# Kernel optimization log

Measured on AMD Instinct MI355X. Metric: run time of the kernel, lower is better.

Reference implementation:

```python
import jax, jax.numpy as jnp
import numpy as np

N_QUBITS = 10
N_LAYERS = 2
QSVT_DEGREE = 3
DT_RANK = 5  # n_qubits // 2
PI = np.float32(np.pi)

# ---- batched statevector simulation helpers (wire 0 = most significant, as in pennylane default.qubit) ----

def _apply_1q(s, wire, U):
    # s: (batch,) + (2,)*n complex; U: (batch,2,2) or (2,2)
    s = jnp.moveaxis(s, 1 + wire, 1)
    shp = s.shape
    s2 = s.reshape(shp[0], 2, -1)
    if U.ndim == 3:
        out = jnp.einsum('bij,bjr->bir', U, s2)
    else:
        out = jnp.einsum('ij,bjr->bir', U, s2)
    return jnp.moveaxis(out.reshape(shp), 1, 1 + wire)

def _ry(t):
    c = jnp.cos(t / 2).astype(jnp.complex64)
    s = jnp.sin(t / 2).astype(jnp.complex64)
    return jnp.stack([jnp.stack([c, -s], -1), jnp.stack([s, c], -1)], -2)

def _rz(t):
    e = jnp.exp(-0.5j * jnp.asarray(t).astype(jnp.complex64))
    z = jnp.zeros_like(e)
    return jnp.stack([jnp.stack([e, z], -1), jnp.stack([z, jnp.conj(e)], -1)], -2)

def _rx(t):
    c = jnp.cos(t / 2).astype(jnp.complex64)
    s = (-1j) * jnp.sin(t / 2).astype(jnp.complex64)
    return jnp.stack([jnp.stack([c, s], -1), jnp.stack([s, c], -1)], -2)

def _cnot(s, control, target):
    f = jnp.flip(s, axis=1 + target)
    s0 = jax.lax.index_in_dim(s, 0, axis=1 + control, keepdims=True)
    f1 = jax.lax.index_in_dim(f, 1, axis=1 + control, keepdims=True)
    return jnp.concatenate([s0, f1], axis=1 + control)

def _circuit(h, x, dt, cp, pc):
    """Batched selective QSVT circuit; h,x,dt: (B,n). Returns <Z_i> per wire, (B,n) float32."""
    n = N_QUBITS
    b = h.shape[0]
    s = jnp.zeros((b, 2 ** n), jnp.complex64).at[:, 0].set(1.0).reshape((b,) + (2,) * n)
    # 1. state encoding
    for i in range(n):
        s = _apply_1q(s, i, _ry(h[:, i]))
    # 2. delta-modulated QSVT block
    for d in range(QSVT_DEGREE + 1):
        for i in range(n):
            s = _apply_1q(s, i, _rz(pc[d] * dt[:, i] * PI))
        for i in range(n - 1):
            s = _cnot(s, i, i + 1)
        s = _cnot(s, n - 1, 0)
    # 3. variational block
    k = 0
    for _ in range(N_LAYERS):
        for i in range(n):
            s = _apply_1q(s, i, _rx(cp[k]))
            s = _apply_1q(s, i, _ry(cp[k + 1]))
            s = _apply_1q(s, i, _rz(cp[k + 2]))
            k += 3
        for i in range(n - 1):
            s = _cnot(s, i, i + 1)
    # 4. delta-modulated input encoding
    for i in range(n):
        s = _apply_1q(s, i, _ry(x[:, i] * dt[:, i]))
    # 5. <Z_i> measurements
    p = s.real ** 2 + s.imag ** 2
    zs = [(jax.lax.index_in_dim(p, 0, 1 + i, False) - jax.lax.index_in_dim(p, 1, 1 + i, False)).reshape(b, -1).sum(-1) for i in range(n)]
    return jnp.stack(zs, -1).astype(jnp.float32)

def setup_inputs() -> dict:
    key = jax.random.key(0)
    ks = jax.random.split(key, 6)
    B, S, n, r = 128, 512, N_QUBITS, DT_RANK
    angles = jax.random.uniform(ks[0], (B, S, n), jnp.float32) * PI  # angle encoding in [0, pi]
    W_x = jax.random.normal(ks[1], (r + 2 * n, n), jnp.float32) * 0.3  # x_proj weight (no bias)
    W_dt = jax.random.normal(ks[2], (n, r), jnp.float32) * 0.3  # dt_proj weight
    rng = np.random.default_rng(0)
    dt0 = np.exp(rng.random(n) * (np.log(0.1) - np.log(0.001)) + np.log(0.001))
    b_dt = jnp.asarray(dt0 + np.log(-np.expm1(-dt0)), jnp.float32)  # inverse-softplus init
    poly_coeffs = jax.random.normal(ks[3], (QSVT_DEGREE + 1,), jnp.float32) * 0.1
    circuit_params = jax.random.normal(ks[4], (n * N_LAYERS * 3,), jnp.float32) * 0.1
    D = jnp.ones((n,), jnp.float32)
    return {"angles": angles, "W_x": W_x, "W_dt": W_dt, "b_dt": b_dt,
            "poly_coeffs": poly_coeffs, "circuit_params": circuit_params, "D": D}

def reference(angles, W_x, W_dt, b_dt, poly_coeffs, circuit_params, D):
    # selective projections
    x_dbc = jnp.einsum('bsn,kn->bsk', angles, W_x)
    dt_raw = x_dbc[..., :DT_RANK]
    # B slice (x_dbc[..., DT_RANK:DT_RANK+n]) is computed but unused in the original forward
    C = x_dbc[..., DT_RANK + N_QUBITS:]
    dt = jax.nn.softplus(jnp.einsum('bsr,nr->bsn', dt_raw, W_dt) + b_dt)
    dt_angles = jnp.tanh(dt) * PI
    # quantum recurrence uses detached tensors in the original (torch .detach())
    x_sg = jax.lax.stop_gradient(angles)
    dt_sg = jax.lax.stop_gradient(dt_angles)
    cp = jax.lax.stop_gradient(circuit_params)
    pc = jax.lax.stop_gradient(poly_coeffs)

    def step(h, xs):
        x_t, d_t = xs
        h2 = _circuit(h, x_t, d_t, cp, pc)
        return h2, h2

    h0 = jnp.zeros((angles.shape[0], N_QUBITS), jnp.float32)
    _, hs = jax.lax.scan(step, h0, (jnp.swapaxes(x_sg, 0, 1), jnp.swapaxes(dt_sg, 0, 1)))
    hs = jnp.swapaxes(hs, 0, 1)  # (B,S,n)
    return C * hs + D * angles
```

## Files before the change

kernel.cpp:

```cpp
#include <hip/hip_runtime.h>
#include <math.h>


#define PIF 3.14159265358979323846f

constexpr int NQ = 10, SEQ = 512, NB = 128, NTHR = 512, RECF = 36;

struct CTbl { int mz[4][NQ]; };
constexpr CTbl build_tbl() {
  CTbl t{};
  unsigned mrow[NQ];
  for (int b = 0; b < NQ; ++b) mrow[b] = 1u << b;
  for (int d = 0; d < 4; ++d) {
    for (int i = 0; i < NQ; ++i) t.mz[d][i] = (int)mrow[9 - i];
    for (int i = 0; i < NQ - 1; ++i) { int bc = 9 - i, bt = 8 - i; mrow[bt] ^= mrow[bc]; }
    mrow[9] ^= mrow[0];
  }
  return t;
}
constexpr CTbl CT = build_tbl();

struct PermCols { int c4[10]; int cL[10]; };
constexpr PermCols build_perms() {
  PermCols P{};
  for (int b = 0; b < 10; ++b) {
    int x = 1 << b;
    for (int d = 0; d < 4; ++d) {
      for (int i = 0; i < 9; ++i) { int bc = 9 - i, bt = 8 - i; if ((x >> bc) & 1) x ^= (1 << bt); }
      if (x & 1) x ^= (1 << 9);
    }
    P.c4[b] = x;
    int y = 1 << b;
    for (int i = 0; i < 9; ++i) { int bc = 9 - i, bt = 8 - i; if ((y >> bc) & 1) y ^= (1 << bt); }
    P.cL[b] = y;
  }
  return P;
}
constexpr PermCols PC = build_perms();

constexpr int lanePart(int x)  { return ((x >> 0) & 1) | (((x >> 5) & 1) << 1) |
                                        (((x >> 1) & 1) << 2) | (((x >> 7) & 1) << 3) |
                                        (((x >> 3) & 1) << 4) | (((x >> 9) & 1) << 5); }
constexpr int wavePart8(int x) { return ((x >> 4) & 1) | (((x >> 8) & 1) << 1) |
                                        (((x >> 6) & 1) << 2); }

typedef __attribute__((ext_vector_type(2))) float v2;

constexpr int VOFS[8] = {0, 16, 256, 272, 64, 80, 320, 336};

template<int C>
__device__ __forceinline__ int dpp1(int x) {
  return __builtin_amdgcn_update_dpp(x, x, C, 0xF, 0xF, false);
}
template<int VL>
__device__ __forceinline__ int lxi(int x) {
  if constexpr (VL == 1)  return dpp1<0xB1>(x);
  else if constexpr (VL == 2)  return dpp1<0x4E>(x);
  else if constexpr (VL == 3)  return dpp1<0x1B>(x);
  else if constexpr (VL <= 7) {
    constexpr int q = (VL & 3) ^ 3;
    int y = x;
    if constexpr (q == 1) y = dpp1<0xB1>(y);
    else if constexpr (q == 2) y = dpp1<0x4E>(y);
    else if constexpr (q == 3) y = dpp1<0x1B>(y);
    return dpp1<0x141>(y);
  } else if constexpr (VL >= 12) {
    constexpr int q = (VL & 3) ^ 3;
    int y = x;
    if constexpr (q == 1) y = dpp1<0xB1>(y);
    else if constexpr (q == 2) y = dpp1<0x4E>(y);
    else if constexpr (q == 3) y = dpp1<0x1B>(y);
    return dpp1<0x140>(y);
  } else {
    constexpr int a = VL & 3;
    int y = x;
    if constexpr (a == 1) y = dpp1<0xB1>(y);
    else if constexpr (a == 2) y = dpp1<0x4E>(y);
    else if constexpr (a == 3) y = dpp1<0x1B>(y);
    y = dpp1<0x141>(y);
    return dpp1<0x140>(y);
  }
}
template<int VL>
__device__ __forceinline__ float lx(float x) {
  if constexpr (VL == 0) return x;
  else if constexpr (VL & 32) {
    int addr = (((int)threadIdx.x & 63) ^ VL) << 2;
    return __int_as_float(__builtin_amdgcn_ds_bpermute(addr, __float_as_int(x)));
  } else if constexpr (VL & 16) {
    return __int_as_float(__builtin_amdgcn_ds_swizzle(__float_as_int(x), (VL << 10) | 0x1F));
  } else {
    return __int_as_float(lxi<VL>(__float_as_int(x)));
  }
}
__device__ __forceinline__ float rdl(float x, int l) {
  return __int_as_float(__builtin_amdgcn_readlane(__float_as_int(x), l));
}

__device__ __forceinline__ int swz(int j) {
  return j ^ (((j >> 5) & 1) << 2) ^ ((j >> 7) & 1);
}

__device__ __forceinline__ void apply2(v2* amp, const v2* p, bool par, float4 U0, float4 U1) {
  v2 u00 = {U0.x, U0.y}, u01 = {U0.z, U0.w}, u10 = {U1.x, U1.y}, u11 = {U1.z, U1.w};
  v2 A = par ? u11 : u00, B = par ? u10 : u01;
  v2 An = {-A.y, A.y}, Bn = {-B.y, B.y};
#pragma unroll
  for (int r = 0; r < 2; ++r) {
    v2 o = amp[r], q = p[r];
    v2 res = A.x * o;
    res += An * __builtin_shufflevector(o, o, 1, 0);
    res += B.x * q;
    res += Bn * __builtin_shufflevector(q, q, 1, 0);
    amp[r] = res;
  }
}

template<int VL>
__device__ __forceinline__ void gate_lane2(v2* amp, float4 U0, float4 U1, int lane) {
  v2 p[2];
#pragma unroll
  for (int r = 0; r < 2; ++r) { p[r].x = lx<VL>(amp[r].x); p[r].y = lx<VL>(amp[r].y); }
  apply2(amp, p, (lane & VL) != 0, U0, U1);
}

__device__ __forceinline__ void gate_reg1(v2* amp, float4 U0, float4 U1) {
  v2 u00 = {U0.x, U0.y}, u01 = {U0.z, U0.w}, u10 = {U1.x, U1.y}, u11 = {U1.z, U1.w};
  v2 o0 = amp[0], o1 = amp[1];
  v2 a0 = {0.f, 0.f}, a1 = {0.f, 0.f};
  a0.x += u00.x * o0.x - u00.y * o0.y;  a0.y += u00.x * o0.y + u00.y * o0.x;
  a0.x += u01.x * o1.x - u01.y * o1.y;  a0.y += u01.x * o1.y + u01.y * o1.x;
  a1.x += u10.x * o0.x - u10.y * o0.y;  a1.y += u10.x * o0.y + u10.y * o0.x;
  a1.x += u11.x * o1.x - u11.y * o1.y;  a1.y += u11.x * o1.y + u11.y * o1.x;
  amp[0] = a0; amp[1] = a1;
}

template<int VL>
__device__ __forceinline__ float xdot_lane2(const v2* amp) {
  v2 acc = {0.f, 0.f};
#pragma unroll
  for (int r = 0; r < 2; ++r) {
    v2 p; p.x = lx<VL>(amp[r].x); p.y = lx<VL>(amp[r].y);
    acc += amp[r] * p;
  }
  return acc.x + acc.y;
}

__global__ __launch_bounds__(NTHR, 2) void qmamba_main(
    const float* __restrict__ angles, const float* __restrict__ Wx,
    const float* __restrict__ Wdt, const float* __restrict__ bdt,
    const float* __restrict__ pc, const float* __restrict__ cp,
    float* __restrict__ out)
{
  __shared__ float  tblL[SEQ][RECF];
  __shared__ float4 uuL[40];
  __shared__ v2     ex0[1024];
  __shared__ v2     ex1[1024];
  __shared__ float  zb[8][16];

  const int tid  = threadIdx.x;
  const int lane = tid & 63;
  const int wave = tid >> 6;
  const int b    = blockIdx.x;

  if (tid < 20) {
    int k = tid * 3;
    float al = 0.5f * cp[k], be = 0.5f * cp[k + 1], ga = 0.5f * cp[k + 2];
    float ca = __cosf(al), sa = __sinf(al);
    float cb = __cosf(be), sb = __sinf(be);
    float cg = __cosf(ga), sg = __sinf(ga);
    float2 M00 = make_float2(cb * ca,  sb * sa);
    float2 M01 = make_float2(-sb * ca, -cb * sa);
    float2 M10 = make_float2(sb * ca,  -cb * sa);
    float2 M11 = make_float2(cb * ca,  -sb * sa);
    float2 e0 = make_float2(cg, -sg), e1 = make_float2(cg, sg);
    auto cm = [](float2 a, float2 c) {
      return make_float2(a.x * c.x - a.y * c.y, a.x * c.y + a.y * c.x);
    };
    float2 u00 = cm(M00, e0), u01 = cm(M01, e0), u10 = cm(M10, e1), u11 = cm(M11, e1);
    uuL[2 * tid]     = make_float4(u00.x, u00.y, u01.x, u01.y);
    uuL[2 * tid + 1] = make_float4(u10.x, u10.y, u11.x, u11.y);
  }

  {
    const int t = tid;
    const float* ar = angles + (size_t)(b * SEQ + t) * NQ;
    float a[NQ];
#pragma unroll
    for (int n = 0; n < NQ; ++n) a[n] = ar[n];
    float dtr[5];
#pragma unroll
    for (int r = 0; r < 5; ++r) {
      float acc = 0.f;
#pragma unroll
      for (int n = 0; n < NQ; ++n) acc += a[n] * Wx[r * NQ + n];
      dtr[r] = acc;
    }
    float* rec = &tblL[t][0];
#pragma unroll
    for (int w = 0; w < NQ; ++w) {
      float lin = bdt[w];
#pragma unroll
      for (int r = 0; r < 5; ++r) lin += dtr[r] * Wdt[w * 5 + r];
      float sp = lin > 0.f ? lin + log1pf(__expf(-lin)) : log1pf(__expf(lin));
      float th = tanhf(sp) * PIF;
      float fa = a[w] * th;
      rec[w]      = th;
      rec[12 + w] = __cosf(fa);
      rec[24 + w] = __sinf(fa);
    }
  }
  __syncthreads();

  float pch[4];
#pragma unroll
  for (int d = 0; d < 4; ++d) pch[d] = 0.5f * pc[d] * PIF;

  v2 cw0[8], cw1[8];
  {
    const int s5 = wave & 1, s1 = (wave >> 1) & 1, s3 = (wave >> 2) & 1;
    auto ent = [&](int g, int row, int col) -> v2 {
      float4 R = uuL[2 * g + row];
      return col ? v2{R.z, R.w} : v2{R.x, R.y};
    };
    auto cmul = [](v2 a, v2 c) -> v2 {
      return v2{a.x * c.x - a.y * c.y, a.x * c.y + a.y * c.x};
    };
#pragma unroll
    for (int v = 0; v < 8; ++v) {
      const int v5 = v & 1, v1 = (v >> 1) & 1, v3 = (v >> 2) & 1;
      cw0[v] = cmul(cmul(ent(5,  s5, s5 ^ v5), ent(1,  s1, s1 ^ v1)), ent(3,  s3, s3 ^ v3));
      cw1[v] = cmul(cmul(ent(15, s5, s5 ^ v5), ent(11, s1, s1 ^ v1)), ent(13, s3, s3 ^ v3));
    }
  }

  unsigned PW0 = 0, PW1 = 0;
#pragma unroll
  for (int k = 0; k < 40; ++k) {
    const int m  = CT.mz[k / 10][k % 10];
    const int lm = lanePart(m), wm = wavePart8(m);
    unsigned flip = ((unsigned)((__popc(lane & lm) ^ __popc(wave & wm)) & 1)) ^ 1u;
    if (k < 32) PW0 |= flip << k; else PW1 |= flip << (k - 32);
  }

  int d4 = 0, dL = 0;
  if (lane & 1)  { d4 ^= PC.c4[0]; dL ^= PC.cL[0]; }
  if (lane & 2)  { d4 ^= PC.c4[5]; dL ^= PC.cL[5]; }
  if (lane & 4)  { d4 ^= PC.c4[1]; dL ^= PC.cL[1]; }
  if (lane & 8)  { d4 ^= PC.c4[7]; dL ^= PC.cL[7]; }
  if (lane & 16) { d4 ^= PC.c4[3]; dL ^= PC.cL[3]; }
  if (lane & 32) { d4 ^= PC.c4[9]; dL ^= PC.cL[9]; }
  if (wave & 1)  { d4 ^= PC.c4[4]; dL ^= PC.cL[4]; }
  if (wave & 2)  { d4 ^= PC.c4[8]; dL ^= PC.cL[8]; }
  if (wave & 4)  { d4 ^= PC.c4[6]; dL ^= PC.cL[6]; }
  const int oR4 = PC.c4[2], oRL = PC.cL[2];

  const int oidx = (lane & 1) | (((lane >> 1) & 1) << 5) | (((lane >> 2) & 1) << 1)
                 | (((lane >> 3) & 1) << 7) | (((lane >> 4) & 1) << 3) | (((lane >> 5) & 1) << 9)
                 | ((wave & 1) << 4) | (((wave >> 1) & 1) << 8) | (((wave >> 2) & 1) << 6);

  float hcw[NQ], hsw[NQ];
#pragma unroll
  for (int w = 0; w < NQ; ++w) { hcw[w] = 1.f; hsw[w] = 0.f; }

  v2 amp[2];

#pragma unroll 1
  for (int t = 0; t < SEQ; ++t) {
    float tha[12];
    {
      const float4* rq = (const float4*)&tblL[t][0];
#pragma unroll
      for (int j = 0; j < 3; ++j) ((float4*)tha)[j] = rq[j];
    }

    float F;
    F  = (lane & 1)  ? hsw[9] : hcw[9];
    F *= (lane & 2)  ? hsw[4] : hcw[4];
    F *= (lane & 4)  ? hsw[8] : hcw[8];
    F *= (lane & 8)  ? hsw[2] : hcw[2];
    F *= (lane & 16) ? hsw[6] : hcw[6];
    F *= (lane & 32) ? hsw[0] : hcw[0];
    F *= (wave & 1)  ? hsw[5] : hcw[5];
    F *= (wave & 2)  ? hsw[1] : hcw[1];
    F *= (wave & 4)  ? hsw[3] : hcw[3];
    const float G0 = F * hcw[7];
    const float G1 = F * hsw[7];

    float S0 = 0.f, S1 = 0.f;
#pragma unroll
    for (int k = 0; k < 40; ++k) {
      const int m  = CT.mz[k / 10][k % 10];
      float v = pch[k / 10] * tha[k % 10];
      unsigned fl = ((k < 32 ? (PW0 >> k) : (PW1 >> (k - 32))) & 1u) << 31;
      float sv = __int_as_float(__float_as_int(v) ^ fl);
      if ((m >> 2) & 1) S1 += sv; else S0 += sv;
    }
    {
      float sn, cs;
      __sincosf(S0 + S1, &sn, &cs); amp[0].x = G0 * cs; amp[0].y = G0 * sn;
      __sincosf(S0 - S1, &sn, &cs); amp[1].x = G1 * cs; amp[1].y = G1 * sn;
    }

    ex0[swz(d4)]       = amp[0];
    ex0[swz(d4 ^ oR4)] = amp[1];
    __syncthreads();
    {
      v2 pv0[8], pv1[8];
#pragma unroll
      for (int v = 0; v < 8; ++v) {
        const int base = oidx ^ VOFS[v];
        pv0[v] = ex0[swz(base)];
        pv1[v] = ex0[swz(base | 4)];
      }
      v2 a0 = {0.f, 0.f}, a1 = {0.f, 0.f};
#pragma unroll
      for (int v = 0; v < 8; ++v) {
        v2 c = cw0[v];
        a0.x += c.x * pv0[v].x - c.y * pv0[v].y;
        a0.y += c.x * pv0[v].y + c.y * pv0[v].x;
        a1.x += c.x * pv1[v].x - c.y * pv1[v].y;
        a1.y += c.x * pv1[v].y + c.y * pv1[v].x;
      }
      amp[0] = a0; amp[1] = a1;
    }
    gate_lane2<32>(amp, uuL[0],  uuL[1],  lane);
    gate_lane2<8> (amp, uuL[4],  uuL[5],  lane);
    gate_lane2<2> (amp, uuL[8],  uuL[9],  lane);
    gate_lane2<16>(amp, uuL[12], uuL[13], lane);
    gate_reg1     (amp, uuL[14], uuL[15]);
    gate_lane2<4> (amp, uuL[16], uuL[17], lane);
    gate_lane2<1> (amp, uuL[18], uuL[19], lane);

    ex1[swz(dL)]       = amp[0];
    ex1[swz(dL ^ oRL)] = amp[1];
    __syncthreads();
    {
      v2 pv0[8], pv1[8];
#pragma unroll
      for (int v = 0; v < 8; ++v) {
        const int base = oidx ^ VOFS[v];
        pv0[v] = ex1[swz(base)];
        pv1[v] = ex1[swz(base | 4)];
      }
      v2 a0 = {0.f, 0.f}, a1 = {0.f, 0.f};
#pragma unroll
      for (int v = 0; v < 8; ++v) {
        v2 c = cw1[v];
        a0.x += c.x * pv0[v].x - c.y * pv0[v].y;
        a0.y += c.x * pv0[v].y + c.y * pv0[v].x;
        a1.x += c.x * pv1[v].x - c.y * pv1[v].y;
        a1.y += c.x * pv1[v].y + c.y * pv1[v].x;
      }
      amp[0] = a0; amp[1] = a1;
    }
    gate_lane2<32>(amp, uuL[20], uuL[21], lane);
    gate_lane2<8> (amp, uuL[24], uuL[25], lane);
    gate_lane2<2> (amp, uuL[28], uuL[29], lane);
    gate_lane2<16>(amp, uuL[32], uuL[33], lane);
    gate_reg1     (amp, uuL[34], uuL[35]);
    gate_lane2<4> (amp, uuL[36], uuL[37], lane);
    gate_lane2<1> (amp, uuL[38], uuL[39], lane);

    ex0[swz(dL)]       = amp[0];
    ex0[swz(dL ^ oRL)] = amp[1];
    __syncthreads();
    v2 pw5[2], pw1[2], pw3[2];
    amp[0] = ex0[swz(oidx)];
    amp[1] = ex0[swz(oidx | 4)];
    pw5[0] = ex0[swz(oidx ^ 16)];   pw5[1] = ex0[swz((oidx ^ 16) | 4)];
    pw1[0] = ex0[swz(oidx ^ 256)];  pw1[1] = ex0[swz((oidx ^ 256) | 4)];
    pw3[0] = ex0[swz(oidx ^ 64)];   pw3[1] = ex0[swz((oidx ^ 64) | 4)];

    float cfv[12], sfv[12];
    {
      const float4* rq = (const float4*)&tblL[t][0];
#pragma unroll
      for (int j = 0; j < 3; ++j) { ((float4*)cfv)[j] = rq[3 + j]; ((float4*)sfv)[j] = rq[6 + j]; }
    }

    const float n0 = amp[0].x * amp[0].x + amp[0].y * amp[0].y;
    const float n1 = amp[1].x * amp[1].x + amp[1].y * amp[1].y;
    const float T0 = n0 + n1;
    const float T1 = n0 - n1;

    auto vdot2 = [](const v2* a, const v2* p) {
      v2 acc = a[0] * p[0] + a[1] * p[1];
      return acc.x + acc.y;
    };

    float zv[NQ];
    { float zp = (lane & 32) ? -T0 : T0; zv[0] = cfv[0] * zp - sfv[0] * xdot_lane2<32>(amp); }
    { float zp = (wave & 2)  ? -T0 : T0; zv[1] = cfv[1] * zp - sfv[1] * vdot2(amp, pw1); }
    { float zp = (lane & 8)  ? -T0 : T0; zv[2] = cfv[2] * zp - sfv[2] * xdot_lane2<8>(amp); }
    { float zp = (wave & 4)  ? -T0 : T0; zv[3] = cfv[3] * zp - sfv[3] * vdot2(amp, pw3); }
    { float zp = (lane & 2)  ? -T0 : T0; zv[4] = cfv[4] * zp - sfv[4] * xdot_lane2<2>(amp); }
    { float zp = (wave & 1)  ? -T0 : T0; zv[5] = cfv[5] * zp - sfv[5] * vdot2(amp, pw5); }
    { float zp = (lane & 16) ? -T0 : T0; zv[6] = cfv[6] * zp - sfv[6] * xdot_lane2<16>(amp); }
    { float xr = 2.f * (amp[0].x * amp[1].x + amp[0].y * amp[1].y);
      zv[7] = cfv[7] * T1 - sfv[7] * xr; }
    { float zp = (lane & 4)  ? -T0 : T0; zv[8] = cfv[8] * zp - sfv[8] * xdot_lane2<4>(amp); }
    { float zp = (lane & 1)  ? -T0 : T0; zv[9] = cfv[9] * zp - sfv[9] * xdot_lane2<1>(amp); }

#pragma unroll
    for (int w = 0; w < NQ; ++w) {
      zv[w] += lx<1>(zv[w]);
      zv[w] += lx<2>(zv[w]);
      zv[w] += lx<4>(zv[w]);
    }
    const int l7 = lane & 7;
    float c01 = (l7 & 1) ? zv[1] : zv[0];
    float c23 = (l7 & 1) ? zv[3] : zv[2];
    float c45 = (l7 & 1) ? zv[5] : zv[4];
    float c67 = (l7 & 1) ? zv[7] : zv[6];
    float c03 = (l7 & 2) ? c23 : c01;
    float c47 = (l7 & 2) ? c67 : c45;
    float pk  = (l7 & 4) ? c47 : c03;
    pk += lx<8>(pk);  pk += lx<16>(pk);  pk += lx<32>(pk);
    float z8 = zv[8]; z8 += lx<8>(z8); z8 += lx<16>(z8); z8 += lx<32>(z8);
    float z9 = zv[9]; z9 += lx<8>(z9); z9 += lx<16>(z9); z9 += lx<32>(z9);
    float zsel = pk;
    zsel = (lane == 8) ? z8 : zsel;
    zsel = (lane == 9) ? z9 : zsel;

    if (lane < NQ) zb[wave][lane] = zsel;
    __syncthreads();
    float z = 0.f;
    if (lane < NQ) {
      z = zb[0][lane] + zb[1][lane] + zb[2][lane] + zb[3][lane]
        + zb[4][lane] + zb[5][lane] + zb[6][lane] + zb[7][lane];
      if (wave == 0) out[(size_t)(b * SEQ + t) * NQ + lane] = z;
    }
    float sn_h, cs_h;
    __sincosf(0.5f * z, &sn_h, &cs_h);
#pragma unroll
    for (int w = 0; w < NQ; ++w) { hcw[w] = rdl(cs_h, w); hsw[w] = rdl(sn_h, w); }
  }
}

__global__ __launch_bounds__(256) void qmamba_post(
    const float* __restrict__ angles, const float* __restrict__ Wx,
    const float* __restrict__ Dg, float* __restrict__ out)
{
  int i = blockIdx.x * 256 + threadIdx.x;
  if (i >= NB * SEQ * NQ) return;
  int w  = i % NQ;
  int bt = i / NQ;
  const float* a = angles + (size_t)bt * NQ;
  float C = 0.f;
#pragma unroll
  for (int n = 0; n < NQ; ++n) C += a[n] * Wx[(15 + w) * NQ + n];
  float z = out[i];
  out[i] = C * z + Dg[w] * a[w];
}

extern "C" void kernel_launch(void* const* d_in, const int* in_sizes, int n_in,
                              void* d_out, int out_size, void* d_ws, size_t ws_size,
                              hipStream_t stream) {
  (void)in_sizes; (void)n_in; (void)out_size; (void)d_ws; (void)ws_size;
  const float* angles = (const float*)d_in[0];
  const float* Wx     = (const float*)d_in[1];
  const float* Wdt    = (const float*)d_in[2];
  const float* bdt    = (const float*)d_in[3];
  const float* pc     = (const float*)d_in[4];
  const float* cp     = (const float*)d_in[5];
  const float* Dg     = (const float*)d_in[6];
  float* out = (float*)d_out;
  hipLaunchKernelGGL(qmamba_main, dim3(NB), dim3(NTHR), 0, stream,
                     angles, Wx, Wdt, bdt, pc, cp, out);
  hipLaunchKernelGGL(qmamba_post, dim3((NB * SEQ * NQ + 255) / 256), dim3(256), 0, stream,
                     angles, Wx, Dg, out);
}
```

Baseline: 2.221 ms.

## Pack two batch elements per block and remap LDS exchange to float4 reads

Each block now runs two independent batch elements with 1024 threads (64 blocks instead of 128), each half using its own LDS exchange buffers and reduction slots. The shared-memory exchange layout is remapped with a new bit permutation and swizzle, so every thread reads both of its amplitudes with a single float4 load instead of two v2 loads. The per-step table is packed tighter (30 floats per step) and read as float2. Intent is fewer LDS instructions per step; the cost is that block-wide barriers now also stall the other element's waves, and there are fewer blocks to spread across CUs.

Result: slower. 7.337 ms (+230.3%).

```diff
diff --git a/kernel.cpp b/kernel.cpp
--- a/kernel.cpp
+++ b/kernel.cpp
@@ -4,7 +4,7 @@
 
 #define PIF 3.14159265358979323846f
 
-constexpr int NQ = 10, SEQ = 512, NB = 128, NTHR = 512, RECF = 36;
+constexpr int NQ = 10, SEQ = 512, NBATCH = 128, NTHR = 1024, NBLK = 64;
 
 struct CTbl { int mz[4][NQ]; };
 constexpr CTbl build_tbl() {
@@ -44,9 +44,18 @@
 constexpr int wavePart8(int x) { return ((x >> 4) & 1) | (((x >> 8) & 1) << 1) |
                                         (((x >> 6) & 1) << 2); }
 
+constexpr int kmap(int x) {
+  return ((x >> 2) & 1)
+       | (((x >> 0) & 1) << 1) | (((x >> 5) & 1) << 2) | (((x >> 1) & 1) << 3)
+       | (((x >> 7) & 1) << 4) | (((x >> 3) & 1) << 5) | (((x >> 9) & 1) << 6)
+       | (((x >> 4) & 1) << 7) | (((x >> 8) & 1) << 8) | (((x >> 6) & 1) << 9);
+}
+constexpr int swzk(int k) { return k ^ (((k >> 5) & 1) << 1) ^ (((k >> 4) & 1) << 2); }
+
+constexpr int SKC4 = swzk(kmap(PC.c4[2]));
+constexpr int SKCL = swzk(kmap(PC.cL[2]));
+
 typedef __attribute__((ext_vector_type(2))) float v2;
-
-constexpr int VOFS[8] = {0, 16, 256, 272, 64, 80, 320, 336};
 
 template<int C>
 __device__ __forceinline__ int dpp1(int x) {
@@ -97,10 +106,6 @@
   return __int_as_float(__builtin_amdgcn_readlane(__float_as_int(x), l));
 }
 
-__device__ __forceinline__ int swz(int j) {
-  return j ^ (((j >> 5) & 1) << 2) ^ ((j >> 7) & 1);
-}
-
 __device__ __forceinline__ void apply2(v2* amp, const v2* p, bool par, float4 U0, float4 U1) {
   v2 u00 = {U0.x, U0.y}, u01 = {U0.z, U0.w}, u10 = {U1.x, U1.y}, u11 = {U1.z, U1.w};
   v2 A = par ? u11 : u00, B = par ? u10 : u01;
@@ -127,11 +132,11 @@
 __device__ __forceinline__ void gate_reg1(v2* amp, float4 U0, float4 U1) {
   v2 u00 = {U0.x, U0.y}, u01 = {U0.z, U0.w}, u10 = {U1.x, U1.y}, u11 = {U1.z, U1.w};
   v2 o0 = amp[0], o1 = amp[1];
-  v2 a0 = {0.f, 0.f}, a1 = {0.f, 0.f};
-  a0.x += u00.x * o0.x - u00.y * o0.y;  a0.y += u00.x * o0.y + u00.y * o0.x;
-  a0.x += u01.x * o1.x - u01.y * o1.y;  a0.y += u01.x * o1.y + u01.y * o1.x;
-  a1.x += u10.x * o0.x - u10.y * o0.y;  a1.y += u10.x * o0.y + u10.y * o0.x;
-  a1.x += u11.x * o1.x - u11.y * o1.y;  a1.y += u11.x * o1.y + u11.y * o1.x;
+  v2 a0, a1;
+  a0.x = u00.x * o0.x - u00.y * o0.y + u01.x * o1.x - u01.y * o1.y;
+  a0.y = u00.x * o0.y + u00.y * o0.x + u01.x * o1.y + u01.y * o1.x;
+  a1.x = u10.x * o0.x - u10.y * o0.y + u11.x * o1.x - u11.y * o1.y;
+  a1.y = u10.x * o0.y + u10.y * o0.x + u11.x * o1.y + u11.y * o1.x;
   amp[0] = a0; amp[1] = a1;
 }
 
@@ -146,22 +151,23 @@
   return acc.x + acc.y;
 }
 
-__global__ __launch_bounds__(NTHR, 2) void qmamba_main(
+__global__ __launch_bounds__(NTHR) void qmamba_main(
     const float* __restrict__ angles, const float* __restrict__ Wx,
     const float* __restrict__ Wdt, const float* __restrict__ bdt,
     const float* __restrict__ pc, const float* __restrict__ cp,
     float* __restrict__ out)
 {
-  __shared__ float  tblL[SEQ][RECF];
+  __shared__ __align__(16) float tbl[2][SEQ][30];
   __shared__ float4 uuL[40];
-  __shared__ v2     ex0[1024];
-  __shared__ v2     ex1[1024];
-  __shared__ float  zb[8][16];
+  __shared__ __align__(16) v2 ex[2][2][1024];
+  __shared__ float  zb[2][8][16];
 
   const int tid  = threadIdx.x;
   const int lane = tid & 63;
   const int wave = tid >> 6;
-  const int b    = blockIdx.x;
+  const int el   = wave >> 3;
+  const int wv   = wave & 7;
+  const int bel  = blockIdx.x * 2 + el;
 
   if (tid < 20) {
     int k = tid * 3;
@@ -183,8 +189,9 @@
   }
 
   {
-    const int t = tid;
-    const float* ar = angles + (size_t)(b * SEQ + t) * NQ;
+    const int pel = tid >> 9, t = tid & (SEQ - 1);
+    const int pb  = blockIdx.x * 2 + pel;
+    const float* ar = angles + (size_t)(pb * SEQ + t) * NQ;
     float a[NQ];
 #pragma unroll
     for (int n = 0; n < NQ; ++n) a[n] = ar[n];
@@ -196,7 +203,7 @@
       for (int n = 0; n < NQ; ++n) acc += a[n] * Wx[r * NQ + n];
       dtr[r] = acc;
     }
-    float* rec = &tblL[t][0];
+    float* rec = &tbl[pel][t][0];
 #pragma unroll
     for (int w = 0; w < NQ; ++w) {
       float lin = bdt[w];
@@ -206,8 +213,8 @@
       float th = tanhf(sp) * PIF;
       float fa = a[w] * th;
       rec[w]      = th;
-      rec[12 + w] = __cosf(fa);
-      rec[24 + w] = __sinf(fa);
+      rec[10 + w] = __cosf(fa);
+      rec[20 + w] = __sinf(fa);
     }
   }
   __syncthreads();
@@ -218,7 +225,7 @@
 
   v2 cw0[8], cw1[8];
   {
-    const int s5 = wave & 1, s1 = (wave >> 1) & 1, s3 = (wave >> 2) & 1;
+    const int s5 = wv & 1, s1 = (wv >> 1) & 1, s3 = (wv >> 2) & 1;
     auto ent = [&](int g, int row, int col) -> v2 {
       float4 R = uuL[2 * g + row];
       return col ? v2{R.z, R.w} : v2{R.x, R.y};
@@ -239,25 +246,26 @@
   for (int k = 0; k < 40; ++k) {
     const int m  = CT.mz[k / 10][k % 10];
     const int lm = lanePart(m), wm = wavePart8(m);
-    unsigned flip = ((unsigned)((__popc(lane & lm) ^ __popc(wave & wm)) & 1)) ^ 1u;
+    unsigned flip = ((unsigned)((__popc(lane & lm) ^ __popc(wv & wm)) & 1)) ^ 1u;
     if (k < 32) PW0 |= flip << k; else PW1 |= flip << (k - 32);
   }
 
-  int d4 = 0, dL = 0;
-  if (lane & 1)  { d4 ^= PC.c4[0]; dL ^= PC.cL[0]; }
-  if (lane & 2)  { d4 ^= PC.c4[5]; dL ^= PC.cL[5]; }
-  if (lane & 4)  { d4 ^= PC.c4[1]; dL ^= PC.cL[1]; }
-  if (lane & 8)  { d4 ^= PC.c4[7]; dL ^= PC.cL[7]; }
-  if (lane & 16) { d4 ^= PC.c4[3]; dL ^= PC.cL[3]; }
-  if (lane & 32) { d4 ^= PC.c4[9]; dL ^= PC.cL[9]; }
-  if (wave & 1)  { d4 ^= PC.c4[4]; dL ^= PC.cL[4]; }
-  if (wave & 2)  { d4 ^= PC.c4[8]; dL ^= PC.cL[8]; }
-  if (wave & 4)  { d4 ^= PC.c4[6]; dL ^= PC.cL[6]; }
-  const int oR4 = PC.c4[2], oRL = PC.cL[2];
-
-  const int oidx = (lane & 1) | (((lane >> 1) & 1) << 5) | (((lane >> 2) & 1) << 1)
-                 | (((lane >> 3) & 1) << 7) | (((lane >> 4) & 1) << 3) | (((lane >> 5) & 1) << 9)
-                 | ((wave & 1) << 4) | (((wave >> 1) & 1) << 8) | (((wave >> 2) & 1) << 6);
+  int d4k = 0, dLk = 0;
+  if (lane & 1)  { d4k ^= kmap(PC.c4[0]); dLk ^= kmap(PC.cL[0]); }
+  if (lane & 2)  { d4k ^= kmap(PC.c4[5]); dLk ^= kmap(PC.cL[5]); }
+  if (lane & 4)  { d4k ^= kmap(PC.c4[1]); dLk ^= kmap(PC.cL[1]); }
+  if (lane & 8)  { d4k ^= kmap(PC.c4[7]); dLk ^= kmap(PC.cL[7]); }
+  if (lane & 16) { d4k ^= kmap(PC.c4[3]); dLk ^= kmap(PC.cL[3]); }
+  if (lane & 32) { d4k ^= kmap(PC.c4[9]); dLk ^= kmap(PC.cL[9]); }
+  if (wv & 1)    { d4k ^= kmap(PC.c4[4]); dLk ^= kmap(PC.cL[4]); }
+  if (wv & 2)    { d4k ^= kmap(PC.c4[8]); dLk ^= kmap(PC.cL[8]); }
+  if (wv & 4)    { d4k ^= kmap(PC.c4[6]); dLk ^= kmap(PC.cL[6]); }
+  const int sd4  = swzk(d4k);
+  const int sdL  = swzk(dLk);
+  const int sown = swzk((lane << 1) | (wv << 7));
+
+  v2* const exA = &ex[el][0][0];
+  v2* const exB = &ex[el][1][0];
 
   float hcw[NQ], hsw[NQ];
 #pragma unroll
@@ -267,11 +275,11 @@
 
 #pragma unroll 1
   for (int t = 0; t < SEQ; ++t) {
-    float tha[12];
-    {
-      const float4* rq = (const float4*)&tblL[t][0];
-#pragma unroll
-      for (int j = 0; j < 3; ++j) ((float4*)tha)[j] = rq[j];
+    float thv[10];
+    {
+      const float2* rq = (const float2*)&tbl[el][t][0];
+#pragma unroll
+      for (int j = 0; j < 5; ++j) { float2 q = rq[j]; thv[2 * j] = q.x; thv[2 * j + 1] = q.y; }
     }
 
     float F;
@@ -281,9 +289,9 @@
     F *= (lane & 8)  ? hsw[2] : hcw[2];
     F *= (lane & 16) ? hsw[6] : hcw[6];
     F *= (lane & 32) ? hsw[0] : hcw[0];
-    F *= (wave & 1)  ? hsw[5] : hcw[5];
-    F *= (wave & 2)  ? hsw[1] : hcw[1];
-    F *= (wave & 4)  ? hsw[3] : hcw[3];
+    F *= (wv & 1)    ? hsw[5] : hcw[5];
+    F *= (wv & 2)    ? hsw[1] : hcw[1];
+    F *= (wv & 4)    ? hsw[3] : hcw[3];
     const float G0 = F * hcw[7];
     const float G1 = F * hsw[7];
 
@@ -291,7 +299,7 @@
 #pragma unroll
     for (int k = 0; k < 40; ++k) {
       const int m  = CT.mz[k / 10][k % 10];
-      float v = pch[k / 10] * tha[k % 10];
+      float v = pch[k / 10] * thv[k % 10];
       unsigned fl = ((k < 32 ? (PW0 >> k) : (PW1 >> (k - 32))) & 1u) << 31;
       float sv = __int_as_float(__float_as_int(v) ^ fl);
       if ((m >> 2) & 1) S1 += sv; else S0 += sv;
@@ -302,25 +310,18 @@
       __sincosf(S0 - S1, &sn, &cs); amp[1].x = G1 * cs; amp[1].y = G1 * sn;
     }
 
-    ex0[swz(d4)]       = amp[0];
-    ex0[swz(d4 ^ oR4)] = amp[1];
+    exA[sd4]        = amp[0];
+    exA[sd4 ^ SKC4] = amp[1];
     __syncthreads();
     {
-      v2 pv0[8], pv1[8];
+      const float4* q4 = (const float4*)exA;
+      v2 a0 = {0.f, 0.f}, a1 = {0.f, 0.f};
 #pragma unroll
       for (int v = 0; v < 8; ++v) {
-        const int base = oidx ^ VOFS[v];
-        pv0[v] = ex0[swz(base)];
-        pv1[v] = ex0[swz(base | 4)];
-      }
-      v2 a0 = {0.f, 0.f}, a1 = {0.f, 0.f};
-#pragma unroll
-      for (int v = 0; v < 8; ++v) {
+        float4 q = q4[(sown ^ (v << 7)) >> 1];
         v2 c = cw0[v];
-        a0.x += c.x * pv0[v].x - c.y * pv0[v].y;
-        a0.y += c.x * pv0[v].y + c.y * pv0[v].x;
-        a1.x += c.x * pv1[v].x - c.y * pv1[v].y;
-        a1.y += c.x * pv1[v].y + c.y * pv1[v].x;
+        a0.x += c.x * q.x - c.y * q.y;  a0.y += c.x * q.y + c.y * q.x;
+        a1.x += c.x * q.z - c.y * q.w;  a1.y += c.x * q.w + c.y * q.z;
       }
       amp[0] = a0; amp[1] = a1;
     }
@@ -332,25 +333,18 @@
     gate_lane2<4> (amp, uuL[16], uuL[17], lane);
     gate_lane2<1> (amp, uuL[18], uuL[19], lane);
 
-    ex1[swz(dL)]       = amp[0];
-    ex1[swz(dL ^ oRL)] = amp[1];
+    exB[sdL]        = amp[0];
+    exB[sdL ^ SKCL] = amp[1];
     __syncthreads();
     {
-      v2 pv0[8], pv1[8];
+      const float4* q4 = (const float4*)exB;
+      v2 a0 = {0.f, 0.f}, a1 = {0.f, 0.f};
 #pragma unroll
       for (int v = 0; v < 8; ++v) {
-        const int base = oidx ^ VOFS[v];
-        pv0[v] = ex1[swz(base)];
-        pv1[v] = ex1[swz(base | 4)];
-      }
-      v2 a0 = {0.f, 0.f}, a1 = {0.f, 0.f};
-#pragma unroll
-      for (int v = 0; v < 8; ++v) {
+        float4 q = q4[(sown ^ (v << 7)) >> 1];
         v2 c = cw1[v];
-        a0.x += c.x * pv0[v].x - c.y * pv0[v].y;
-        a0.y += c.x * pv0[v].y + c.y * pv0[v].x;
-        a1.x += c.x * pv1[v].x - c.y * pv1[v].y;
-        a1.y += c.x * pv1[v].y + c.y * pv1[v].x;
+        a0.x += c.x * q.x - c.y * q.y;  a0.y += c.x * q.y + c.y * q.x;
+        a1.x += c.x * q.z - c.y * q.w;  a1.y += c.x * q.w + c.y * q.z;
       }
       amp[0] = a0; amp[1] = a1;
     }
@@ -362,21 +356,31 @@
     gate_lane2<4> (amp, uuL[36], uuL[37], lane);
     gate_lane2<1> (amp, uuL[38], uuL[39], lane);
 
-    ex0[swz(dL)]       = amp[0];
-    ex0[swz(dL ^ oRL)] = amp[1];
+    exA[sdL]        = amp[0];
+    exA[sdL ^ SKCL] = amp[1];
     __syncthreads();
     v2 pw5[2], pw1[2], pw3[2];
-    amp[0] = ex0[swz(oidx)];
-    amp[1] = ex0[swz(oidx | 4)];
-    pw5[0] = ex0[swz(oidx ^ 16)];   pw5[1] = ex0[swz((oidx ^ 16) | 4)];
-    pw1[0] = ex0[swz(oidx ^ 256)];  pw1[1] = ex0[swz((oidx ^ 256) | 4)];
-    pw3[0] = ex0[swz(oidx ^ 64)];   pw3[1] = ex0[swz((oidx ^ 64) | 4)];
-
-    float cfv[12], sfv[12];
-    {
-      const float4* rq = (const float4*)&tblL[t][0];
-#pragma unroll
-      for (int j = 0; j < 3; ++j) { ((float4*)cfv)[j] = rq[3 + j]; ((float4*)sfv)[j] = rq[6 + j]; }
+    {
+      const float4* q4 = (const float4*)exA;
+      float4 qs = q4[sown >> 1];
+      float4 q5 = q4[(sown ^ (1 << 7)) >> 1];
+      float4 q1 = q4[(sown ^ (2 << 7)) >> 1];
+      float4 q3 = q4[(sown ^ (4 << 7)) >> 1];
+      amp[0] = v2{qs.x, qs.y}; amp[1] = v2{qs.z, qs.w};
+      pw5[0] = v2{q5.x, q5.y}; pw5[1] = v2{q5.z, q5.w};
+      pw1[0] = v2{q1.x, q1.y}; pw1[1] = v2{q1.z, q1.w};
+      pw3[0] = v2{q3.x, q3.y}; pw3[1] = v2{q3.z, q3.w};
+    }
+
+    float cfv[10], sfv[10];
+    {
+      const float2* rq = (const float2*)&tbl[el][t][0];
+#pragma unroll
+      for (int j = 0; j < 5; ++j) {
+        float2 qc = rq[5 + j], qsn = rq[10 + j];
+        cfv[2 * j] = qc.x; cfv[2 * j + 1] = qc.y;
+        sfv[2 * j] = qsn.x; sfv[2 * j + 1] = qsn.y;
+      }
     }
 
     const float n0 = amp[0].x * amp[0].x + amp[0].y * amp[0].y;
@@ -391,11 +395,11 @@
 
     float zv[NQ];
     { float zp = (lane & 32) ? -T0 : T0; zv[0] = cfv[0] * zp - sfv[0] * xdot_lane2<32>(amp); }
-    { float zp = (wave & 2)  ? -T0 : T0; zv[1] = cfv[1] * zp - sfv[1] * vdot2(amp, pw1); }
+    { float zp = (wv & 2)    ? -T0 : T0; zv[1] = cfv[1] * zp - sfv[1] * vdot2(amp, pw1); }
     { float zp = (lane & 8)  ? -T0 : T0; zv[2] = cfv[2] * zp - sfv[2] * xdot_lane2<8>(amp); }
-    { float zp = (wave & 4)  ? -T0 : T0; zv[3] = cfv[3] * zp - sfv[3] * vdot2(amp, pw3); }
+    { float zp = (wv & 4)    ? -T0 : T0; zv[3] = cfv[3] * zp - sfv[3] * vdot2(amp, pw3); }
     { float zp = (lane & 2)  ? -T0 : T0; zv[4] = cfv[4] * zp - sfv[4] * xdot_lane2<2>(amp); }
-    { float zp = (wave & 1)  ? -T0 : T0; zv[5] = cfv[5] * zp - sfv[5] * vdot2(amp, pw5); }
+    { float zp = (wv & 1)    ? -T0 : T0; zv[5] = cfv[5] * zp - sfv[5] * vdot2(amp, pw5); }
     { float zp = (lane & 16) ? -T0 : T0; zv[6] = cfv[6] * zp - sfv[6] * xdot_lane2<16>(amp); }
     { float xr = 2.f * (amp[0].x * amp[1].x + amp[0].y * amp[1].y);
       zv[7] = cfv[7] * T1 - sfv[7] * xr; }
@@ -423,13 +427,13 @@
     zsel = (lane == 8) ? z8 : zsel;
     zsel = (lane == 9) ? z9 : zsel;
 
-    if (lane < NQ) zb[wave][lane] = zsel;
+    if (lane < NQ) zb[el][wv][lane] = zsel;
     __syncthreads();
     float z = 0.f;
     if (lane < NQ) {
-      z = zb[0][lane] + zb[1][lane] + zb[2][lane] + zb[3][lane]
-        + zb[4][lane] + zb[5][lane] + zb[6][lane] + zb[7][lane];
-      if (wave == 0) out[(size_t)(b * SEQ + t) * NQ + lane] = z;
+      z = zb[el][0][lane] + zb[el][1][lane] + zb[el][2][lane] + zb[el][3][lane]
+        + zb[el][4][lane] + zb[el][5][lane] + zb[el][6][lane] + zb[el][7][lane];
+      if (wv == 0) out[(size_t)(bel * SEQ + t) * NQ + lane] = z;
     }
     float sn_h, cs_h;
     __sincosf(0.5f * z, &sn_h, &cs_h);
@@ -443,7 +447,7 @@
     const float* __restrict__ Dg, float* __restrict__ out)
 {
   int i = blockIdx.x * 256 + threadIdx.x;
-  if (i >= NB * SEQ * NQ) return;
+  if (i >= NBATCH * SEQ * NQ) return;
   int w  = i % NQ;
   int bt = i / NQ;
   const float* a = angles + (size_t)bt * NQ;
@@ -466,8 +470,8 @@
   const float* cp     = (const float*)d_in[5];
   const float* Dg     = (const float*)d_in[6];
   float* out = (float*)d_out;
-  hipLaunchKernelGGL(qmamba_main, dim3(NB), dim3(NTHR), 0, stream,
+  hipLaunchKernelGGL(qmamba_main, dim3(NBLK), dim3(NTHR), 0, stream,
                      angles, Wx, Wdt, bdt, pc, cp, out);
-  hipLaunchKernelGGL(qmamba_post, dim3((NB * SEQ * NQ + 255) / 256), dim3(256), 0, stream,
+  hipLaunchKernelGGL(qmamba_post, dim3((NBATCH * SEQ * NQ + 255) / 256), dim3(256), 0, stream,
                      angles, Wx, Dg, out);
 }
```
